# Kernel tuning notes

Measured on AMD Instinct MI355X. Metric: run time of the kernel, lower is better.

The kernel has to match this reference:

```python
import jax, jax.numpy as jnp
import numpy as np

EPS = 1e-6
INF = 1e30  # stands in for 'no value' in the sparse C_bar lists of the torch code


def setup_inputs() -> dict:
    key = jax.random.key(0)
    M, N, D = 512, 256, 64
    kx, ky, kq = jax.random.split(key, 3)
    x = jax.random.normal(kx, (M, D), dtype=jnp.float32)
    y = jax.random.normal(ky, (N, D), dtype=jnp.float32)
    u = jax.random.uniform(kq, (N + 1, N), dtype=jnp.float32, minval=0.05, maxval=1.0)
    q = u / jnp.sum(u, axis=0, keepdims=True)  # column-stochastic jump probabilities
    return {"x": x, "y": y, "q": q}


def _pal_forward(x, y, q):
    M, N = x.shape[0], y.shape[0]
    dt = x.dtype

    # ---- compute_dists: pairwise L2 (p=2 norm), M x N ----
    diff = x[:, None, :] - y[None, :, :]
    dists = jnp.sqrt(jnp.sum(diff * diff, axis=2))

    # ---- compute_reachability: sequential accumulation over columns of q ----
    def reach_step(p, nb):
        return p + p[nb] * q[:, nb], None
    p0 = jnp.zeros(N + 1, dtype=dt).at[0].set(1.0)
    p, _ = jax.lax.scan(reach_step, p0, jnp.arange(N))
    p_back = p[:N][None, :] * q / (p[:, None] + EPS)  # (N+1, N)

    # ---- edge structure: ancestors n_bar < n with p_back > 0 (detached mask) ----
    tri = jnp.tril(jnp.ones((N, N), dtype=bool), k=-1)
    E = tri & (jax.lax.stop_gradient(p_back[:N]) > 0)   # (N, N): E[n, n_bar]
    w = jnp.where(E, p_back[:N], 0.0)                   # mixing weights

    ns = jnp.arange(1, N)

    def row_dp(d_row, base0, C_prev, Cbar_prev):
        """One row m of the lattice. C_prev: C[m-1] (N,), Cbar_prev: C_bar[m-1] (N,N).
        Returns C[m] (N,) and C_bar[m] (N,N) with INF at non-edge slots."""
        C0 = jnp.zeros(N, dtype=dt).at[0].set(d_row[0] + base0)

        def n_step(Ccur, n):
            # min over: C[m][n_bar] (insert y), C[m-1][n_bar] (match), C_bar[m-1][n][n_bar] (insert x)
            c_min = jnp.minimum(Ccur, jnp.minimum(C_prev, Cbar_prev[n]))  # (N,) over n_bar
            cbar = d_row[n] + c_min
            val = jnp.sum(jnp.where(E[n], w[n] * cbar, 0.0))
            return Ccur.at[n].set(val), jnp.where(E[n], cbar, INF)

        C_row, Cbar_rows = jax.lax.scan(n_step, C0, ns)
        Cbar = jnp.concatenate([jnp.full((1, N), INF, dt), Cbar_rows], axis=0)
        return C_row, Cbar

    # m = 0: no previous row -> previous-row candidates disabled via INF, C[0][0] = d[0,0]
    C_row0, Cbar0 = row_dp(dists[0], jnp.zeros((), dt), jnp.full(N, INF, dt), jnp.full((N, N), INF, dt))

    def m_step(carry, d_row):
        C_prev, Cbar_prev = carry
        C_row, Cbar = row_dp(d_row, C_prev[0], C_prev, Cbar_prev)  # C[m][0] = d[m,0] + C[m-1][0]
        return (C_row, Cbar), None

    (C_last, _), _ = jax.lax.scan(m_step, (C_row0, Cbar0), dists[1:])

    # expected cost of reaching END from each terminal n
    return jnp.sum(p_back[N] * C_last)


def reference(x, y, q):
    return _pal_forward(x, y, q)
```

## Files before the change

### kernel.cpp

```cpp
#include <hip/hip_runtime.h>

typedef float f4 __attribute__((ext_vector_type(4)));

#define Nn 256
#define Mm 512
#define Dd 64
#define EPSF 1e-6f
#define INFF 1e30f
#define BC 8
#define NCHUNK (Nn / BC)
#define R 16
#define NBLK 8
#define WVS 4
#define SST (NBLK * WVS)
#define SLOTS 4
#define QSTR 260

#define OFF_D     0
#define OFF_QC    131072
#define OFF_P     197632
#define OFF_WT    197892
#define OFF_CBAR  263428
#define OFF_CROW  328964
#define OFF_FLAG  337156

__device__ __forceinline__ int llc_load_int(const int* p) {
  int v;
  asm volatile("global_load_dword %0, %1, off sc0 sc1\n\ts_waitcnt vmcnt(0)"
               : "=v"(v) : "v"(p) : "memory");
  return v;
}
__device__ __forceinline__ void llc_store_int(int* p, int v) {
  asm volatile("global_store_dword %0, %1, off sc0 sc1" :: "v"(p), "v"(v) : "memory");
}
__device__ __forceinline__ void llc_load_cbar10(const float* b0, const float* cp,
                                                f4 c[8], f4& pl, f4& ph) {
  const float* b1 = b0 + 4 * Nn;
  asm volatile(
    "global_load_dwordx4 %0, %10, off sc0 sc1\n\t"
    "global_load_dwordx4 %1, %10, off offset:1024 sc0 sc1\n\t"
    "global_load_dwordx4 %2, %10, off offset:2048 sc0 sc1\n\t"
    "global_load_dwordx4 %3, %10, off offset:3072 sc0 sc1\n\t"
    "global_load_dwordx4 %4, %11, off sc0 sc1\n\t"
    "global_load_dwordx4 %5, %11, off offset:1024 sc0 sc1\n\t"
    "global_load_dwordx4 %6, %11, off offset:2048 sc0 sc1\n\t"
    "global_load_dwordx4 %7, %11, off offset:3072 sc0 sc1\n\t"
    "global_load_dwordx4 %8, %12, off sc0 sc1\n\t"
    "global_load_dwordx4 %9, %12, off offset:16 sc0 sc1\n\t"
    "s_waitcnt vmcnt(0)"
    : "=v"(c[0]), "=v"(c[1]), "=v"(c[2]), "=v"(c[3]),
      "=v"(c[4]), "=v"(c[5]), "=v"(c[6]), "=v"(c[7]),
      "=v"(pl), "=v"(ph)
    : "v"(b0), "v"(b1), "v"(cp)
    : "memory");
}
__device__ __forceinline__ void llc_store_cbar8(float* b0, const f4 c[8]) {
  float* b1 = b0 + 4 * Nn;
  asm volatile(
    "global_store_dwordx4 %8, %0, off sc0 sc1\n\t"
    "global_store_dwordx4 %8, %1, off offset:1024 sc0 sc1\n\t"
    "global_store_dwordx4 %8, %2, off offset:2048 sc0 sc1\n\t"
    "global_store_dwordx4 %8, %3, off offset:3072 sc0 sc1\n\t"
    "global_store_dwordx4 %9, %4, off sc0 sc1\n\t"
    "global_store_dwordx4 %9, %5, off offset:1024 sc0 sc1\n\t"
    "global_store_dwordx4 %9, %6, off offset:2048 sc0 sc1\n\t"
    "global_store_dwordx4 %9, %7, off offset:3072 sc0 sc1\n\t"
    "s_waitcnt vmcnt(0)"
    :: "v"(c[0]), "v"(c[1]), "v"(c[2]), "v"(c[3]),
       "v"(c[4]), "v"(c[5]), "v"(c[6]), "v"(c[7]),
       "v"(b0), "v"(b1)
    : "memory");
}
__device__ __forceinline__ float rdlane(float v, int l) {
  return __int_as_float(__builtin_amdgcn_readlane(__float_as_int(v), l));
}

__global__ __launch_bounds__(256) void k_pre(const float* __restrict__ x,
                                             const float* __restrict__ y,
                                             const float* __restrict__ q,
                                             float* __restrict__ ws) {
  __shared__ float xs[Dd];
  __shared__ float tile[32][33];
  __shared__ float p[257];
  __shared__ float vsnap[64];
  __shared__ float qtile[64][65];
  const int b = blockIdx.x, t = threadIdx.x;
  if (b < Mm) {
    if (t < Dd) xs[t] = x[b * Dd + t];
    __syncthreads();
    const float4* y4 = (const float4*)(y + t * Dd);
    float acc = 0.f;
#pragma unroll
    for (int k = 0; k < Dd / 4; k++) {
      float4 v = y4[k];
      float a0 = xs[4*k+0] - v.x, a1 = xs[4*k+1] - v.y;
      float a2 = xs[4*k+2] - v.z, a3 = xs[4*k+3] - v.w;
      acc += a0*a0 + a1*a1 + a2*a2 + a3*a3;
    }
    ws[OFF_D + b * Nn + t] = sqrtf(acc);
  } else if (b < Mm + 64) {
    const int tb = b - Mm;
    const int t0 = (tb & 7) * 32;
    const int j0 = (tb >> 3) * 32;
    const int tx = t & 31, ty = t >> 5;
#pragma unroll
    for (int dy = 0; dy < 4; dy++)
      tile[ty + 8 * dy][tx] = q[(j0 + ty + 8 * dy) * Nn + t0 + tx];
    __syncthreads();
#pragma unroll
    for (int dy = 0; dy < 4; dy++)
      ws[OFF_QC + (t0 + ty + 8 * dy) * QSTR + j0 + tx] = tile[tx][ty + 8 * dy];
  } else if (b == Mm + 64) {
    ((int*)(ws + OFF_FLAG))[t] = 0;
  } else {
    float* p_out = ws + OFF_P;
    p[t] = (t == 0) ? 1.f : 0.f;
    if (t == 0) p[256] = 0.f;
    __syncthreads();
    for (int g = 0; g < 4; g++) {
      int g0 = g * 64;
      for (int z = 0; z < 16; z++) {
        int idx = t + z * 256, l = idx >> 6, k = idx & 63;
        qtile[k][l] = q[(g0 + l) * Nn + g0 + k];
      }
      __syncthreads();
      if (t < 64) {
        float pv = p[g0 + t];
        for (int k = 0; k < 64; k++) {
          float v = __shfl(pv, k, 64);
          if (t == k) vsnap[k] = v;
          pv += v * qtile[k][t];
        }
      }
      __syncthreads();
      float4 qs[16];
      const float4* qrow = (const float4*)(q + t * Nn + g0);
#pragma unroll
      for (int i = 0; i < 16; i++) qs[i] = qrow[i];
      float acc = p[t];
#pragma unroll
      for (int i = 0; i < 16; i++) {
        acc += vsnap[4*i+0] * qs[i].x;
        acc += vsnap[4*i+1] * qs[i].y;
        acc += vsnap[4*i+2] * qs[i].z;
        acc += vsnap[4*i+3] * qs[i].w;
      }
      float acc2 = 0.f;
      if (t == 0) {
        acc2 = p[256];
        const float4* qlast = (const float4*)(q + 256 * Nn + g0);
#pragma unroll
        for (int i = 0; i < 16; i++) {
          float4 v = qlast[i];
          acc2 += vsnap[4*i+0] * v.x + vsnap[4*i+1] * v.y
                + vsnap[4*i+2] * v.z + vsnap[4*i+3] * v.w;
        }
      }
      __syncthreads();
      p[t] = acc;
      if (t == 0) p[256] = acc2;
      __syncthreads();
    }
    p_out[t] = p[t];
    if (t == 0) p_out[256] = p[256];
  }
}

__global__ __launch_bounds__(256) void k_wbuild(const float* __restrict__ qc, const float* __restrict__ p,
                                                float* __restrict__ wT) {
  int t = blockIdx.x, n = threadIdx.x;
  float v = 0.f;
  if (t < n) v = p[t] * qc[t * QSTR + n] / (p[n] + EPSF);
  wT[t * Nn + n] = v;
}

__global__ __launch_bounds__(256, 1) void k_main(const float* __restrict__ d,
                                                 const float* __restrict__ wT,
                                                 float* __restrict__ cbarG,
                                                 float* __restrict__ crowG,
                                                 int* __restrict__ flags,
                                                 const float* __restrict__ q,
                                                 const float* __restrict__ p,
                                                 float* __restrict__ out) {
  __shared__ __align__(16) float sbuf[SLOTS][BC * Nn];
  __shared__ __align__(16) float crow_lds[WVS][SLOTS][BC];
  __shared__ __align__(16) float crow_fin[Nn];

  const int tid  = threadIdx.x;
  const int wave = tid >> 6;
  const int lane = tid & 63;
  const int blk  = blockIdx.x;
  const int stage = blk * WVS + wave;
  const int m0 = stage * R;

  f4 dl[R], S[R];
#pragma unroll
  for (int r = 0; r < R; r++) {
    dl[r] = *(const f4*)(d + (m0 + r) * Nn + 4 * lane);
    S[r] = (f4){0.f, 0.f, 0.f, 0.f};
  }
  f4 Wt = (f4){0.f, 0.f, 0.f, 0.f};
#pragma unroll 8
  for (int t = 0; t < Nn; t++)
    Wt += *(const f4*)(wT + t * Nn + 4 * lane);

#pragma clang loop unroll(disable)
  for (int s = 0; s < NCHUNK + WVS - 1; s++) {
    const int j = s - wave;
    if (j >= 0 && j < NCHUNK) {
      f4 wv[BC];
#pragma unroll
      for (int tt = 0; tt < BC; tt++)
        wv[tt] = *(const f4*)(wT + (j * BC + tt) * Nn + 4 * lane);

      f4 c[BC], cpl, cph;
      float* lsl = &sbuf[j & (SLOTS - 1)][0] + 4 * lane;

      if (wave == 0) {
        if (blk > 0) {
          const int* fp = flags + (blk - 1) * NCHUNK + j;
          while (llc_load_int(fp) == 0) __builtin_amdgcn_s_sleep(1);
          llc_load_cbar10(cbarG + (size_t)j * BC * Nn + 4 * lane,
                          crowG + (blk - 1) * Nn + j * BC, c, cpl, cph);
        } else {
          cpl = (f4){INFF, INFF, INFF, INFF};
          cph = cpl;
#pragma unroll
          for (int tt = 0; tt < BC; tt++) c[tt] = cpl;
        }
      } else {
#pragma unroll
        for (int tt = 0; tt < BC; tt++) c[tt] = *(const f4*)(lsl + tt * Nn);
        const float* cr = &crow_lds[wave - 1][j & (SLOTS - 1)][0];
        cpl = *(const f4*)cr;
        cph = *(const f4*)(cr + 4);
      }

      f4 clast4;
      const bool isJ0 = (j == 0);
#pragma unroll
      for (int tt = 0; tt < BC; tt++) {
        const int owner = 2 * j + (tt >> 2);
        const int comp = tt & 3;
        const bool isT0 = isJ0 && (tt == 0);

        float up = (tt < 4) ? cpl[comp] : cph[comp];
        float prcMin = up;
        float prcVal = up;
        if (isT0 && stage == 0) prcVal = 0.f;
        float cml[R];
#pragma unroll
        for (int r = 0; r < R; r++) {
          float Cv;
          if (isT0) Cv = dl[r][0] + prcVal;
          else      Cv = fmaf(dl[r][comp], Wt[comp], S[r][comp]);
          cml[r] = fminf(Cv, prcMin);
          prcVal = Cv;
          prcMin = Cv;
        }
        float cmB[R];
#pragma unroll
        for (int r = 0; r < R; r++) cmB[r] = rdlane(cml[r], owner);
        float clastv = rdlane(prcVal, owner);
        if (lane == owner) clast4[comp] = clastv;

#pragma unroll
        for (int k = 0; k < 4; k++) {
          const float w_ = wv[tt][k];
          float cbv = c[tt][k];
#pragma unroll
          for (int r = 0; r < R; r++) {
            float a = fminf(cmB[r], cbv);
            S[r][k] = fmaf(w_, a, S[r][k]);
            cbv = dl[r][k] + a;
          }
          c[tt][k] = (w_ > 0.f) ? cbv : c[tt][k];
        }
      }

      if (wave < WVS - 1) {
#pragma unroll
        for (int tt = 0; tt < BC; tt++) *(f4*)(lsl + tt * Nn) = c[tt];
        if (lane == 2 * j || lane == 2 * j + 1)
          *(f4*)&crow_lds[wave][j & (SLOTS - 1)][(lane & 1) * 4] = clast4;
      } else if (blk < NBLK - 1) {
        if (lane == 2 * j || lane == 2 * j + 1) {
          float* cp = crowG + blk * Nn + j * BC + (lane & 1) * 4;
          asm volatile("global_store_dwordx4 %0, %1, off sc0 sc1" :: "v"(cp), "v"(clast4) : "memory");
        }
        llc_store_cbar8(cbarG + (size_t)j * BC * Nn + 4 * lane, c);
        if (lane == 0) llc_store_int(flags + blk * NCHUNK + j, 1);
      } else {
        if (lane == 2 * j || lane == 2 * j + 1)
          *(f4*)&crow_fin[j * BC + (lane & 1) * 4] = clast4;
      }
    }
    __syncthreads();
  }

  if (blk == NBLK - 1) {
    float fw = p[tid] * q[Nn * Nn + tid] / (p[Nn] + EPSF);
    crow_fin[tid] *= fw;
    __syncthreads();
    for (int sft = 128; sft > 0; sft >>= 1) {
      if (tid < sft) crow_fin[tid] += crow_fin[tid + sft];
      __syncthreads();
    }
    if (tid == 0) out[0] = crow_fin[0];
  }
}

extern "C" void kernel_launch(void* const* d_in, const int* in_sizes, int n_in,
                              void* d_out, int out_size, void* d_ws, size_t ws_size,
                              hipStream_t stream) {
  const float* x = (const float*)d_in[0];
  const float* y = (const float*)d_in[1];
  const float* q = (const float*)d_in[2];
  float* ws = (float*)d_ws;
  float* out = (float*)d_out;
  hipLaunchKernelGGL(k_pre,   dim3(Mm + 64 + 2), dim3(256), 0, stream, x, y, q, ws);
  hipLaunchKernelGGL(k_wbuild,dim3(Nn),  dim3(256), 0, stream, ws + OFF_QC, ws + OFF_P,
                     ws + OFF_WT);
  hipLaunchKernelGGL(k_main,  dim3(NBLK), dim3(256), 0, stream, ws + OFF_D, ws + OFF_WT,
                     ws + OFF_CBAR, ws + OFF_CROW, (int*)(ws + OFF_FLAG),
                     q, ws + OFF_P, out);
}
```

Before: 403.5 us.

## Add dedicated prefetch wave for cross-block C_bar handoff and defer flag stores

Adds a fifth wave per block that polls the upstream block's flags and loads the next chunk of C_bar and C-row data from global memory into a double-buffered LDS staging area, so the first compute wave no longer spins and waits on global loads inside its critical path. The last compute wave now issues its C_bar stores without waiting on completion and publishes each chunk's flag one pipeline step later, relying on the intervening barriers and later waits for visibility. This is meant to hide inter-block handoff latency in the wavefront pipeline, at the cost of an extra wave, more LDS and a subtler memory-ordering argument for the delayed flag publication.

```diff
diff --git a/kernel.cpp b/kernel.cpp
--- a/kernel.cpp
+++ b/kernel.cpp
@@ -11,8 +11,8 @@
 #define NCHUNK (Nn / BC)
 #define R 16
 #define NBLK 8
-#define WVS 4
-#define SST (NBLK * WVS)
+#define CW 4
+#define SST (NBLK * CW)
 #define SLOTS 4
 #define QSTR 260
 
@@ -54,7 +54,7 @@
     : "v"(b0), "v"(b1), "v"(cp)
     : "memory");
 }
-__device__ __forceinline__ void llc_store_cbar8(float* b0, const f4 c[8]) {
+__device__ __forceinline__ void llc_store_cbar8_nw(float* b0, const f4 c[8]) {
   float* b1 = b0 + 4 * Nn;
   asm volatile(
     "global_store_dwordx4 %8, %0, off sc0 sc1\n\t"
@@ -64,8 +64,7 @@
     "global_store_dwordx4 %9, %4, off sc0 sc1\n\t"
     "global_store_dwordx4 %9, %5, off offset:1024 sc0 sc1\n\t"
     "global_store_dwordx4 %9, %6, off offset:2048 sc0 sc1\n\t"
-    "global_store_dwordx4 %9, %7, off offset:3072 sc0 sc1\n\t"
-    "s_waitcnt vmcnt(0)"
+    "global_store_dwordx4 %9, %7, off offset:3072 sc0 sc1"
     :: "v"(c[0]), "v"(c[1]), "v"(c[2]), "v"(c[3]),
        "v"(c[4]), "v"(c[5]), "v"(c[6]), "v"(c[7]),
        "v"(b0), "v"(b1)
@@ -174,7 +173,7 @@
   wT[t * Nn + n] = v;
 }
 
-__global__ __launch_bounds__(256, 1) void k_main(const float* __restrict__ d,
+__global__ __launch_bounds__(320, 1) void k_main(const float* __restrict__ d,
                                                  const float* __restrict__ wT,
                                                  float* __restrict__ cbarG,
                                                  float* __restrict__ crowG,
@@ -183,124 +182,162 @@
                                                  const float* __restrict__ p,
                                                  float* __restrict__ out) {
   __shared__ __align__(16) float sbuf[SLOTS][BC * Nn];
-  __shared__ __align__(16) float crow_lds[WVS][SLOTS][BC];
+  __shared__ __align__(16) float stg[2][BC * Nn];
+  __shared__ __align__(16) float stg_cr[2][8];
+  __shared__ __align__(16) float crow_lds[CW][SLOTS][BC];
   __shared__ __align__(16) float crow_fin[Nn];
 
   const int tid  = threadIdx.x;
   const int wave = tid >> 6;
   const int lane = tid & 63;
   const int blk  = blockIdx.x;
-  const int stage = blk * WVS + wave;
+  const int stage = blk * CW + wave;
   const int m0 = stage * R;
 
-  f4 dl[R], S[R];
-#pragma unroll
-  for (int r = 0; r < R; r++) {
-    dl[r] = *(const f4*)(d + (m0 + r) * Nn + 4 * lane);
-    S[r] = (f4){0.f, 0.f, 0.f, 0.f};
-  }
-  f4 Wt = (f4){0.f, 0.f, 0.f, 0.f};
+  f4 dl[R], S[R], Wt;
+  if (wave < CW) {
+#pragma unroll
+    for (int r = 0; r < R; r++) {
+      dl[r] = *(const f4*)(d + (m0 + r) * Nn + 4 * lane);
+      S[r] = (f4){0.f, 0.f, 0.f, 0.f};
+    }
+    Wt = (f4){0.f, 0.f, 0.f, 0.f};
 #pragma unroll 8
-  for (int t = 0; t < Nn; t++)
-    Wt += *(const f4*)(wT + t * Nn + 4 * lane);
+    for (int t = 0; t < Nn; t++)
+      Wt += *(const f4*)(wT + t * Nn + 4 * lane);
+  }
+
+  if (wave == CW && blk > 0) {
+    const int* fp = flags + (blk - 1) * NCHUNK;
+    while (llc_load_int(fp) == 0) __builtin_amdgcn_s_sleep(1);
+    f4 c0[BC], pl, ph;
+    llc_load_cbar10(cbarG + 4 * lane, crowG + (blk - 1) * Nn, c0, pl, ph);
+#pragma unroll
+    for (int tt = 0; tt < BC; tt++) *(f4*)&stg[0][tt * Nn + 4 * lane] = c0[tt];
+    if (lane == 0) { *(f4*)&stg_cr[0][0] = pl; *(f4*)&stg_cr[0][4] = ph; }
+  }
+  __syncthreads();
 
 #pragma clang loop unroll(disable)
-  for (int s = 0; s < NCHUNK + WVS - 1; s++) {
-    const int j = s - wave;
-    if (j >= 0 && j < NCHUNK) {
-      f4 wv[BC];
-#pragma unroll
-      for (int tt = 0; tt < BC; tt++)
-        wv[tt] = *(const f4*)(wT + (j * BC + tt) * Nn + 4 * lane);
-
-      f4 c[BC], cpl, cph;
-      float* lsl = &sbuf[j & (SLOTS - 1)][0] + 4 * lane;
-
-      if (wave == 0) {
-        if (blk > 0) {
-          const int* fp = flags + (blk - 1) * NCHUNK + j;
-          while (llc_load_int(fp) == 0) __builtin_amdgcn_s_sleep(1);
-          llc_load_cbar10(cbarG + (size_t)j * BC * Nn + 4 * lane,
-                          crowG + (blk - 1) * Nn + j * BC, c, cpl, cph);
+  for (int s = 0; s < NCHUNK + CW - 1; s++) {
+    if (wave < CW) {
+      if (wave == CW - 1 && blk < NBLK - 1 && s >= 4 && lane == 0)
+        llc_store_int(flags + blk * NCHUNK + (s - 4), 1);
+
+      const int j = s - wave;
+      if (j >= 0 && j < NCHUNK) {
+        f4 wv[BC];
+#pragma unroll
+        for (int tt = 0; tt < BC; tt++)
+          wv[tt] = *(const f4*)(wT + (j * BC + tt) * Nn + 4 * lane);
+
+        f4 c[BC], cpl, cph;
+        float* lsl = &sbuf[j & (SLOTS - 1)][0] + 4 * lane;
+
+        if (wave == 0) {
+          if (blk > 0) {
+#pragma unroll
+            for (int tt = 0; tt < BC; tt++) c[tt] = *(const f4*)&stg[j & 1][tt * Nn + 4 * lane];
+            cpl = *(const f4*)&stg_cr[j & 1][0];
+            cph = *(const f4*)&stg_cr[j & 1][4];
+          } else {
+            cpl = (f4){INFF, INFF, INFF, INFF};
+            cph = cpl;
+#pragma unroll
+            for (int tt = 0; tt < BC; tt++) c[tt] = cpl;
+          }
         } else {
-          cpl = (f4){INFF, INFF, INFF, INFF};
-          cph = cpl;
-#pragma unroll
-          for (int tt = 0; tt < BC; tt++) c[tt] = cpl;
-        }
-      } else {
-#pragma unroll
-        for (int tt = 0; tt < BC; tt++) c[tt] = *(const f4*)(lsl + tt * Nn);
-        const float* cr = &crow_lds[wave - 1][j & (SLOTS - 1)][0];
-        cpl = *(const f4*)cr;
-        cph = *(const f4*)(cr + 4);
-      }
-
-      f4 clast4;
-      const bool isJ0 = (j == 0);
-#pragma unroll
-      for (int tt = 0; tt < BC; tt++) {
-        const int owner = 2 * j + (tt >> 2);
-        const int comp = tt & 3;
-        const bool isT0 = isJ0 && (tt == 0);
-
-        float up = (tt < 4) ? cpl[comp] : cph[comp];
-        float prcMin = up;
-        float prcVal = up;
-        if (isT0 && stage == 0) prcVal = 0.f;
-        float cml[R];
-#pragma unroll
-        for (int r = 0; r < R; r++) {
-          float Cv;
-          if (isT0) Cv = dl[r][0] + prcVal;
-          else      Cv = fmaf(dl[r][comp], Wt[comp], S[r][comp]);
-          cml[r] = fminf(Cv, prcMin);
-          prcVal = Cv;
-          prcMin = Cv;
-        }
-        float cmB[R];
-#pragma unroll
-        for (int r = 0; r < R; r++) cmB[r] = rdlane(cml[r], owner);
-        float clastv = rdlane(prcVal, owner);
-        if (lane == owner) clast4[comp] = clastv;
-
-#pragma unroll
-        for (int k = 0; k < 4; k++) {
-          const float w_ = wv[tt][k];
-          float cbv = c[tt][k];
+#pragma unroll
+          for (int tt = 0; tt < BC; tt++) c[tt] = *(const f4*)(lsl + tt * Nn);
+          const float* cr = &crow_lds[wave - 1][j & (SLOTS - 1)][0];
+          cpl = *(const f4*)cr;
+          cph = *(const f4*)(cr + 4);
+        }
+
+        f4 clast4;
+        const bool isJ0 = (j == 0);
+#pragma unroll
+        for (int tt = 0; tt < BC; tt++) {
+          const int owner = 2 * j + (tt >> 2);
+          const int comp = tt & 3;
+          const bool isT0 = isJ0 && (tt == 0);
+
+          float up = (tt < 4) ? cpl[comp] : cph[comp];
+          float prcMin = up;
+          float prcVal = up;
+          if (isT0 && stage == 0) prcVal = 0.f;
+          float cml[R];
 #pragma unroll
           for (int r = 0; r < R; r++) {
-            float a = fminf(cmB[r], cbv);
-            S[r][k] = fmaf(w_, a, S[r][k]);
-            cbv = dl[r][k] + a;
+            float Cv;
+            if (isT0) Cv = dl[r][0] + prcVal;
+            else      Cv = fmaf(dl[r][comp], Wt[comp], S[r][comp]);
+            cml[r] = fminf(Cv, prcMin);
+            prcVal = Cv;
+            prcMin = Cv;
           }
-          c[tt][k] = (w_ > 0.f) ? cbv : c[tt][k];
-        }
-      }
-
-      if (wave < WVS - 1) {
-#pragma unroll
-        for (int tt = 0; tt < BC; tt++) *(f4*)(lsl + tt * Nn) = c[tt];
-        if (lane == 2 * j || lane == 2 * j + 1)
-          *(f4*)&crow_lds[wave][j & (SLOTS - 1)][(lane & 1) * 4] = clast4;
-      } else if (blk < NBLK - 1) {
-        if (lane == 2 * j || lane == 2 * j + 1) {
-          float* cp = crowG + blk * Nn + j * BC + (lane & 1) * 4;
-          asm volatile("global_store_dwordx4 %0, %1, off sc0 sc1" :: "v"(cp), "v"(clast4) : "memory");
-        }
-        llc_store_cbar8(cbarG + (size_t)j * BC * Nn + 4 * lane, c);
-        if (lane == 0) llc_store_int(flags + blk * NCHUNK + j, 1);
-      } else {
-        if (lane == 2 * j || lane == 2 * j + 1)
-          *(f4*)&crow_fin[j * BC + (lane & 1) * 4] = clast4;
-      }
-    }
-    __syncthreads();
+          float cmB[R];
+#pragma unroll
+          for (int r = 0; r < R; r++) cmB[r] = rdlane(cml[r], owner);
+          float clastv = rdlane(prcVal, owner);
+          if (lane == owner) clast4[comp] = clastv;
+
+#pragma unroll
+          for (int k = 0; k < 4; k++) {
+            const float w_ = wv[tt][k];
+            float cbv = c[tt][k];
+#pragma unroll
+            for (int r = 0; r < R; r++) {
+              float a = fminf(cmB[r], cbv);
+              S[r][k] = fmaf(w_, a, S[r][k]);
+              cbv = dl[r][k] + a;
+            }
+            c[tt][k] = (w_ > 0.f) ? cbv : c[tt][k];
+          }
+        }
+
+        if (wave < CW - 1) {
+#pragma unroll
+          for (int tt = 0; tt < BC; tt++) *(f4*)(lsl + tt * Nn) = c[tt];
+          if (lane == 2 * j || lane == 2 * j + 1)
+            *(f4*)&crow_lds[wave][j & (SLOTS - 1)][(lane & 1) * 4] = clast4;
+        } else if (blk < NBLK - 1) {
+          if (lane == 2 * j || lane == 2 * j + 1) {
+            float* cp = crowG + blk * Nn + j * BC + (lane & 1) * 4;
+            asm volatile("global_store_dwordx4 %0, %1, off sc0 sc1" :: "v"(cp), "v"(clast4) : "memory");
+          }
+          llc_store_cbar8_nw(cbarG + (size_t)j * BC * Nn + 4 * lane, c);
+        } else {
+          if (lane == 2 * j || lane == 2 * j + 1)
+            *(f4*)&crow_fin[j * BC + (lane & 1) * 4] = clast4;
+        }
+      }
+    } else {
+      const int jn = s + 1;
+      if (blk > 0 && jn < NCHUNK) {
+        const int* fp = flags + (blk - 1) * NCHUNK + jn;
+        while (llc_load_int(fp) == 0) __builtin_amdgcn_s_sleep(1);
+        f4 cn[BC], pl, ph;
+        llc_load_cbar10(cbarG + (size_t)jn * BC * Nn + 4 * lane,
+                        crowG + (blk - 1) * Nn + jn * BC, cn, pl, ph);
+#pragma unroll
+        for (int tt = 0; tt < BC; tt++) *(f4*)&stg[jn & 1][tt * Nn + 4 * lane] = cn[tt];
+        if (lane == 0) { *(f4*)&stg_cr[jn & 1][0] = pl; *(f4*)&stg_cr[jn & 1][4] = ph; }
+      }
+    }
+    __syncthreads();
+  }
+
+  if (wave == CW - 1 && blk < NBLK - 1 && lane == 0) {
+    asm volatile("s_waitcnt vmcnt(0)" ::: "memory");
+    llc_store_int(flags + blk * NCHUNK + (NCHUNK - 1), 1);
   }
 
   if (blk == NBLK - 1) {
-    float fw = p[tid] * q[Nn * Nn + tid] / (p[Nn] + EPSF);
-    crow_fin[tid] *= fw;
+    if (tid < Nn) {
+      float fw = p[tid] * q[Nn * Nn + tid] / (p[Nn] + EPSF);
+      crow_fin[tid] *= fw;
+    }
     __syncthreads();
     for (int sft = 128; sft > 0; sft >>= 1) {
       if (tid < sft) crow_fin[tid] += crow_fin[tid + sft];
@@ -321,7 +358,7 @@
   hipLaunchKernelGGL(k_pre,   dim3(Mm + 64 + 2), dim3(256), 0, stream, x, y, q, ws);
   hipLaunchKernelGGL(k_wbuild,dim3(Nn),  dim3(256), 0, stream, ws + OFF_QC, ws + OFF_P,
                      ws + OFF_WT);
-  hipLaunchKernelGGL(k_main,  dim3(NBLK), dim3(256), 0, stream, ws + OFF_D, ws + OFF_WT,
+  hipLaunchKernelGGL(k_main,  dim3(NBLK), dim3(320), 0, stream, ws + OFF_D, ws + OFF_WT,
                      ws + OFF_CBAR, ws + OFF_CROW, (int*)(ws + OFF_FLAG),
                      q, ws + OFF_P, out);
 }
```

New measurement: 813.9 us. +101.7%, slower.

## Prefetch next inter-block C_bar chunk into LDS via async global-to-LDS DMA

Applied to the files above, without the earlier changes.

Wave 0 of each block no longer polls the flag and loads a chunk from the previous block at the moment it needs it. It now waits on the flag for chunk j+1 and starts an asynchronous global_load_lds copy into a double-buffered LDS staging area, while the current chunk is read from LDS. The last-column C values (crow) are packed into the same per-chunk payload as an extra row, so one DMA brings both and the separate crowG buffer goes away. The aim is to hide the cross-block handoff latency behind compute. In exchange, correctness now depends on the async LDS writes completing before the next iteration reads them, which relies on the barrier's implicit wait.

```diff
diff --git a/kernel.cpp b/kernel.cpp
--- a/kernel.cpp
+++ b/kernel.cpp
@@ -8,6 +8,7 @@
 #define EPSF 1e-6f
 #define INFF 1e30f
 #define BC 8
+#define PROW (BC + 1)
 #define NCHUNK (Nn / BC)
 #define R 16
 #define NBLK 8
@@ -15,13 +16,13 @@
 #define SST (NBLK * WVS)
 #define SLOTS 4
 #define QSTR 260
+#define AUXC 0x11
 
 #define OFF_D     0
 #define OFF_QC    131072
 #define OFF_P     197632
 #define OFF_WT    197892
 #define OFF_CBAR  263428
-#define OFF_CROW  328964
 #define OFF_FLAG  337156
 
 __device__ __forceinline__ int llc_load_int(const int* p) {
@@ -32,27 +33,6 @@
 }
 __device__ __forceinline__ void llc_store_int(int* p, int v) {
   asm volatile("global_store_dword %0, %1, off sc0 sc1" :: "v"(p), "v"(v) : "memory");
-}
-__device__ __forceinline__ void llc_load_cbar10(const float* b0, const float* cp,
-                                                f4 c[8], f4& pl, f4& ph) {
-  const float* b1 = b0 + 4 * Nn;
-  asm volatile(
-    "global_load_dwordx4 %0, %10, off sc0 sc1\n\t"
-    "global_load_dwordx4 %1, %10, off offset:1024 sc0 sc1\n\t"
-    "global_load_dwordx4 %2, %10, off offset:2048 sc0 sc1\n\t"
-    "global_load_dwordx4 %3, %10, off offset:3072 sc0 sc1\n\t"
-    "global_load_dwordx4 %4, %11, off sc0 sc1\n\t"
-    "global_load_dwordx4 %5, %11, off offset:1024 sc0 sc1\n\t"
-    "global_load_dwordx4 %6, %11, off offset:2048 sc0 sc1\n\t"
-    "global_load_dwordx4 %7, %11, off offset:3072 sc0 sc1\n\t"
-    "global_load_dwordx4 %8, %12, off sc0 sc1\n\t"
-    "global_load_dwordx4 %9, %12, off offset:16 sc0 sc1\n\t"
-    "s_waitcnt vmcnt(0)"
-    : "=v"(c[0]), "=v"(c[1]), "=v"(c[2]), "=v"(c[3]),
-      "=v"(c[4]), "=v"(c[5]), "=v"(c[6]), "=v"(c[7]),
-      "=v"(pl), "=v"(ph)
-    : "v"(b0), "v"(b1), "v"(cp)
-    : "memory");
 }
 __device__ __forceinline__ void llc_store_cbar8(float* b0, const f4 c[8]) {
   float* b1 = b0 + 4 * Nn;
@@ -74,6 +54,16 @@
 __device__ __forceinline__ float rdlane(float v, int l) {
   return __int_as_float(__builtin_amdgcn_readlane(__float_as_int(v), l));
 }
+typedef const __attribute__((address_space(1))) float gfloat;
+typedef __attribute__((address_space(3))) float lfloat;
+__device__ __forceinline__ void dma16(const float* g, float* l) {
+  __builtin_amdgcn_global_load_lds((gfloat*)g, (lfloat*)l, 16, 0, AUXC);
+}
+__device__ __forceinline__ void dma_payload(const float* slice, float* stgbuf, int lane) {
+#pragma unroll
+  for (int tt = 0; tt < PROW; tt++)
+    dma16(slice + tt * Nn + 4 * lane, stgbuf + tt * Nn);
+}
 
 __global__ __launch_bounds__(256) void k_pre(const float* __restrict__ x,
                                              const float* __restrict__ y,
@@ -177,12 +167,12 @@
 __global__ __launch_bounds__(256, 1) void k_main(const float* __restrict__ d,
                                                  const float* __restrict__ wT,
                                                  float* __restrict__ cbarG,
-                                                 float* __restrict__ crowG,
                                                  int* __restrict__ flags,
                                                  const float* __restrict__ q,
                                                  const float* __restrict__ p,
                                                  float* __restrict__ out) {
   __shared__ __align__(16) float sbuf[SLOTS][BC * Nn];
+  __shared__ __align__(16) float stg[2][PROW * Nn];
   __shared__ __align__(16) float crow_lds[WVS][SLOTS][BC];
   __shared__ __align__(16) float crow_fin[Nn];
 
@@ -204,6 +194,13 @@
   for (int t = 0; t < Nn; t++)
     Wt += *(const f4*)(wT + t * Nn + 4 * lane);
 
+  if (wave == 0 && blk > 0) {
+    const int* fp = flags + (blk - 1) * NCHUNK;
+    while (llc_load_int(fp) == 0) __builtin_amdgcn_s_sleep(1);
+    dma_payload(cbarG, &stg[0][0], lane);
+  }
+  __syncthreads();
+
 #pragma clang loop unroll(disable)
   for (int s = 0; s < NCHUNK + WVS - 1; s++) {
     const int j = s - wave;
@@ -218,10 +215,16 @@
 
       if (wave == 0) {
         if (blk > 0) {
-          const int* fp = flags + (blk - 1) * NCHUNK + j;
-          while (llc_load_int(fp) == 0) __builtin_amdgcn_s_sleep(1);
-          llc_load_cbar10(cbarG + (size_t)j * BC * Nn + 4 * lane,
-                          crowG + (blk - 1) * Nn + j * BC, c, cpl, cph);
+          const float* sb = &stg[j & 1][0];
+#pragma unroll
+          for (int tt = 0; tt < BC; tt++) c[tt] = *(const f4*)(sb + tt * Nn + 4 * lane);
+          cpl = *(const f4*)(sb + BC * Nn);
+          cph = *(const f4*)(sb + BC * Nn + 4);
+          if (j + 1 < NCHUNK) {
+            const int* fp = flags + (blk - 1) * NCHUNK + (j + 1);
+            while (llc_load_int(fp) == 0) __builtin_amdgcn_s_sleep(1);
+            dma_payload(cbarG + (size_t)(j + 1) * PROW * Nn, &stg[(j + 1) & 1][0], lane);
+          }
         } else {
           cpl = (f4){INFF, INFF, INFF, INFF};
           cph = cpl;
@@ -285,10 +288,10 @@
           *(f4*)&crow_lds[wave][j & (SLOTS - 1)][(lane & 1) * 4] = clast4;
       } else if (blk < NBLK - 1) {
         if (lane == 2 * j || lane == 2 * j + 1) {
-          float* cp = crowG + blk * Nn + j * BC + (lane & 1) * 4;
+          float* cp = cbarG + (size_t)j * PROW * Nn + BC * Nn + (lane & 1) * 4;
           asm volatile("global_store_dwordx4 %0, %1, off sc0 sc1" :: "v"(cp), "v"(clast4) : "memory");
         }
-        llc_store_cbar8(cbarG + (size_t)j * BC * Nn + 4 * lane, c);
+        llc_store_cbar8(cbarG + (size_t)j * PROW * Nn + 4 * lane, c);
         if (lane == 0) llc_store_int(flags + blk * NCHUNK + j, 1);
       } else {
         if (lane == 2 * j || lane == 2 * j + 1)
@@ -322,6 +325,5 @@
   hipLaunchKernelGGL(k_wbuild,dim3(Nn),  dim3(256), 0, stream, ws + OFF_QC, ws + OFF_P,
                      ws + OFF_WT);
   hipLaunchKernelGGL(k_main,  dim3(NBLK), dim3(256), 0, stream, ws + OFF_D, ws + OFF_WT,
-                     ws + OFF_CBAR, ws + OFF_CROW, (int*)(ws + OFF_FLAG),
-                     q, ws + OFF_P, out);
-}
+                     ws + OFF_CBAR, (int*)(ws + OFF_FLAG), q, ws + OFF_P, out);
+}
```

Measured after the change: 427.0 us. +5.8%, slower.
